# Performance work log

Measured on AMD Instinct MI355X. Metric: run time of the kernel, lower is better.

The kernel has to match this reference:

```python
import jax, jax.numpy as jnp
import numpy as np

D_MODEL, D_STATE, D_CONV, EXPAND, N_HEADS = 1024, 64, 4, 2, 8
D_INNER = EXPAND * D_MODEL
D_HEAD = D_INNER // N_HEADS
B, T = 2, 2048
EPS = 1e-6


def setup_inputs() -> dict:
    key = jax.random.key(0)
    ks = jax.random.split(key, 12)
    s = 0.02
    return {
        "x": jax.random.normal(ks[0], (B, T, D_MODEL), jnp.float32),
        "norm_w": jnp.ones((D_MODEL,), jnp.float32),
        "in_w": jax.random.normal(ks[1], (2 * D_INNER, D_MODEL), jnp.float32) * s,
        "conv_w": jax.random.normal(ks[2], (D_INNER, 1, D_CONV), jnp.float32) * s,
        "conv_b": jnp.zeros((D_INNER,), jnp.float32),
        "A_log": jax.random.normal(ks[3], (N_HEADS,), jnp.float32),
        "B_w": jax.random.normal(ks[4], (N_HEADS * D_STATE, D_INNER), jnp.float32) * s,
        "C_w": jax.random.normal(ks[5], (N_HEADS * D_STATE, D_INNER), jnp.float32) * s,
        "dt_w": jax.random.normal(ks[6], (N_HEADS, D_INNER), jnp.float32) * s,
        "dt_b": jnp.zeros((N_HEADS,), jnp.float32),
        "D": jnp.ones((N_HEADS,), jnp.float32),
        "out_w": jax.random.normal(ks[7], (D_MODEL, D_INNER), jnp.float32) * s,
    }


def _rmsnorm(x, w):
    var = jnp.mean(jnp.square(x), axis=-1, keepdims=True)
    return x * jax.lax.rsqrt(var + EPS) * w


def _silu(x):
    return x * jax.nn.sigmoid(x)


def reference(x, norm_w, in_w, conv_w, conv_b, A_log, B_w, C_w, dt_w, dt_b, D, out_w):
    residual = x
    xn = _rmsnorm(x, norm_w)
    xz = xn @ in_w.T                                   # (B,T,2*D_INNER)
    x_ssm, z = jnp.split(xz, 2, axis=-1)

    # causal depthwise conv1d (torch pads both sides by K-1 then slices [:T] == left pad only)
    xc = jnp.transpose(x_ssm, (0, 2, 1))               # (B,C,T)
    xc = jax.lax.conv_general_dilated(
        xc, conv_w, window_strides=(1,), padding=[(D_CONV - 1, 0)],
        feature_group_count=D_INNER,
        dimension_numbers=("NCH", "OIH", "NCH"))
    xc = xc + conv_b[None, :, None]
    x_ssm = _silu(jnp.transpose(xc, (0, 2, 1)))        # (B,T,D_INNER)

    dt = jax.nn.softplus(x_ssm @ dt_w.T + dt_b)        # (B,T,H)
    Bm = (x_ssm @ B_w.T).reshape(B, T, N_HEADS, D_STATE)
    Cm = (x_ssm @ C_w.T).reshape(B, T, N_HEADS, D_STATE)
    xh = x_ssm.reshape(B, T, N_HEADS, D_HEAD)
    A = -jnp.exp(A_log)                                # (H,)

    # time-major for scan
    dt_t = jnp.transpose(dt, (1, 0, 2))                # (T,B,H)
    B_t = jnp.transpose(Bm, (1, 0, 2, 3))              # (T,B,H,N)
    C_t = jnp.transpose(Cm, (1, 0, 2, 3))
    x_t = jnp.transpose(xh, (1, 0, 2, 3))              # (T,B,H,D)

    def step(h, inp):
        dtt, bt, ct, xt = inp
        dA = jnp.exp(dtt * A)[..., None, None]         # (B,H,1,1)
        h = dA * h + dtt[..., None, None] * bt[..., :, None] * xt[..., None, :]
        y = jnp.einsum("bhn,bhnd->bhd", ct, h)
        return h, y

    h0 = jnp.zeros((B, N_HEADS, D_STATE, D_HEAD), x.dtype)
    _, ys = jax.lax.scan(step, h0, (dt_t, B_t, C_t, x_t))  # ys: (T,B,H,D)
    y = jnp.transpose(ys, (1, 0, 2, 3))                # (B,T,H,D)
    y = y + xh * D[None, None, :, None]
    y = y.reshape(B, T, D_INNER)
    y = y * _silu(z)
    out = y @ out_w.T
    return residual + out
```

## Files before the change

### kernel.cpp

```cpp
#include <hip/hip_runtime.h>
#include <hip/hip_bf16.h>
#include <math.h>

#define D_MODEL 1024
#define D_STATE 64
#define D_CONV  4
#define D_INNER 2048
#define N_HEADS 8
#define D_HEAD  256
#define BATCH   2
#define SEQ     2048
#define ROWS    (BATCH*SEQ)
#define NCHUNK  32
#define EPS     1e-6f

typedef __attribute__((ext_vector_type(2))) unsigned short ushort2v;
typedef __attribute__((ext_vector_type(4))) unsigned short ushort4v;
typedef __attribute__((ext_vector_type(8))) unsigned short ushort8v;
typedef __attribute__((ext_vector_type(8))) short short8v;
typedef __attribute__((ext_vector_type(4))) float f32x4;

__device__ __forceinline__ float silu_f(float x){ return x / (1.0f + __expf(-x)); }
__device__ __forceinline__ float softplus_f(float x){ return (x > 20.0f) ? x : log1pf(__expf(x)); }
__device__ __forceinline__ float bf2f(unsigned short u){
    union { unsigned int i; float f; } v; v.i = ((unsigned int)u) << 16; return v.f;
}
__device__ __forceinline__ unsigned short f2bf_bits(float f){
    __hip_bfloat16 h = __float2bfloat16(f);
    return *(unsigned short*)&h;
}
__device__ __forceinline__ void gload_lds16(const void* g, void* l){
    __builtin_amdgcn_global_load_lds((const __attribute__((address_space(1))) void*)g,
                                     (__attribute__((address_space(3))) void*)l, 16, 0, 0);
}
__device__ __forceinline__ void vmw(int n){
    switch(n){
        case 0:  asm volatile("s_waitcnt vmcnt(0)"  ::: "memory"); break;
        case 2:  asm volatile("s_waitcnt vmcnt(2)"  ::: "memory"); break;
        case 3:  asm volatile("s_waitcnt vmcnt(3)"  ::: "memory"); break;
        case 4:  asm volatile("s_waitcnt vmcnt(4)"  ::: "memory"); break;
        case 6:  asm volatile("s_waitcnt vmcnt(6)"  ::: "memory"); break;
        case 8:  asm volatile("s_waitcnt vmcnt(8)"  ::: "memory"); break;
        default: asm volatile("s_waitcnt vmcnt(0)"  ::: "memory"); break;
    }
}

__global__ __launch_bounds__(256) void prep_kernel(const float* __restrict__ in_w,
                                                   const float* __restrict__ out_w,
                                                   const float* __restrict__ B_w,
                                                   const float* __restrict__ C_w,
                                                   unsigned short* __restrict__ inw_bf,
                                                   unsigned short* __restrict__ outw_bf,
                                                   unsigned short* __restrict__ BCw_bf){
    int i = blockIdx.x * 256 + threadIdx.x;
    const float* src; unsigned short* dst; int j;
    if (i < 1048576)      { src = in_w;  dst = inw_bf;            j = i; }
    else if (i < 1572864) { src = out_w; dst = outw_bf;           j = i - 1048576; }
    else if (i < 1835008) { src = B_w;   dst = BCw_bf;            j = i - 1572864; }
    else                  { src = C_w;   dst = BCw_bf + 1048576;  j = i - 1835008; }
    float4 v = ((const float4*)src)[j];
    ushort4v o;
    o[0] = f2bf_bits(v.x); o[1] = f2bf_bits(v.y);
    o[2] = f2bf_bits(v.z); o[3] = f2bf_bits(v.w);
    ((ushort4v*)dst)[j] = o;
}

__global__ __launch_bounds__(256) void rmsnorm_kernel(const float* __restrict__ x,
                                                      const float* __restrict__ w,
                                                      unsigned short* __restrict__ xn){
    int row = blockIdx.x;
    int tid = threadIdx.x;
    const float4* xr = (const float4*)(x + (size_t)row * D_MODEL);
    float4 a = xr[tid];
    float ss = a.x*a.x + a.y*a.y + a.z*a.z + a.w*a.w;
    #pragma unroll
    for (int i = 1; i < 64; i <<= 1) ss += __shfl_xor(ss, i);
    __shared__ float red[4];
    int lane = tid & 63, wid = tid >> 6;
    if (lane == 0) red[wid] = ss;
    __syncthreads();
    float tot = red[0] + red[1] + red[2] + red[3];
    float scale = rsqrtf(tot * (1.0f / D_MODEL) + EPS);
    float4 wv = ((const float4*)w)[tid];
    ushort4v o;
    o[0] = f2bf_bits(a.x * scale * wv.x);
    o[1] = f2bf_bits(a.y * scale * wv.y);
    o[2] = f2bf_bits(a.z * scale * wv.z);
    o[3] = f2bf_bits(a.w * scale * wv.w);
    ((ushort4v*)(xn + (size_t)row * D_MODEL))[tid] = o;
}

__global__ __launch_bounds__(512) void gemm_in512(const unsigned short* __restrict__ A,
                                                  const unsigned short* __restrict__ W,
                                                  unsigned short* __restrict__ Cout0,
                                                  unsigned short* __restrict__ Cout1){
    const int K = D_MODEL;
    __shared__ unsigned short As[2][256*32];
    __shared__ unsigned short Bs[2][128*32];
    int tid = threadIdx.x;
    int bid = blockIdx.x;
    int x = bid & 7;
    int r = bid >> 3;
    int m0 = ((x & 3)*4 + (r >> 4)) * 256;
    int n0 = ((x >> 2)*16 + (r & 15)) * 128;

    int lane = tid & 63;
    int w = tid >> 6;
    int wrow = w >> 1, wcol = w & 1;
    f32x4 acc[4][4];
    #pragma unroll
    for (int i = 0; i < 4; ++i)
        #pragma unroll
        for (int j = 0; j < 4; ++j) acc[i][j] = (f32x4){0.f,0.f,0.f,0.f};

    int g0 = tid >> 3, s0 = tid & 7;
    int swz0 = (s0*16) ^ ((g0&7)<<4);
    int r0 = 2*g0 + (swz0 >> 6);
    int c0e = (swz0 & 63) >> 1;
    const unsigned short* aS0 = A + (size_t)(m0 + r0)*K + c0e;
    const unsigned short* aS1 = aS0 + (size_t)128*K;
    const unsigned short* bS0 = W + (size_t)(n0 + r0)*K + c0e;

    int frow = lane & 15;
    int fkb  = (lane >> 4) * 16;
    int offA[4], offB[4];
    #pragma unroll
    for (int m = 0; m < 4; ++m){
        int rr = wrow*64 + m*16 + frow;
        int lb = (rr&1)*64 + fkb;
        offA[m] = (rr>>1)*128 + (lb ^ (((rr>>1)&7)<<4));
    }
    #pragma unroll
    for (int n = 0; n < 4; ++n){
        int rr = wcol*64 + n*16 + frow;
        int lb = (rr&1)*64 + fkb;
        offB[n] = (rr>>1)*128 + (lb ^ (((rr>>1)&7)<<4));
    }

    #define STAGE(buf, k0) do{ \
        gload_lds16(aS0 + (k0), &As[buf][(size_t)tid*8]); \
        gload_lds16(aS1 + (k0), &As[buf][(size_t)(tid+512)*8]); \
        gload_lds16(bS0 + (k0), &Bs[buf][(size_t)tid*8]); \
    }while(0)

    #define COMPUTE(buf, tt) do{ \
        short8v af[4], bf[4]; \
        _Pragma("unroll") \
        for (int m = 0; m < 4; ++m) af[m] = *(const short8v*)((const char*)As[buf] + offA[m]); \
        _Pragma("unroll") \
        for (int n = 0; n < 4; ++n) bf[n] = *(const short8v*)((const char*)Bs[buf] + offB[n]); \
        asm volatile("s_waitcnt lgkmcnt(0)" ::: "memory"); \
        __builtin_amdgcn_sched_barrier(0); \
        __builtin_amdgcn_s_barrier(); \
        if ((tt) + 2 < NT) STAGE(buf, (size_t)((tt)+2)*32); \
        _Pragma("unroll") \
        for (int m = 0; m < 4; ++m) \
            _Pragma("unroll") \
            for (int n = 0; n < 4; ++n) \
                acc[m][n] = __builtin_amdgcn_mfma_f32_16x16x32_bf16(af[m], bf[n], acc[m][n], 0, 0, 0); \
    }while(0)

    int NT = K >> 5;
    STAGE(0, 0);
    STAGE(1, 32);
    int t = 0;
    for (; t < NT-1; ++t){
        vmw(3);
        __builtin_amdgcn_sched_barrier(0);
        __builtin_amdgcn_s_barrier();
        COMPUTE(t & 1, t);
    }
    {
        vmw(0);
        __builtin_amdgcn_sched_barrier(0);
        __builtin_amdgcn_s_barrier();
        COMPUTE(t & 1, t);
    }
    #undef COMPUTE
    #undef STAGE

    int rrow = (lane >> 4) * 4;
    int rcol = lane & 15;
    unsigned short* outp;
    int colbase;
    if (n0 < 2048){ outp = Cout0; colbase = n0; }
    else          { outp = Cout1; colbase = n0 - 2048; }
    #pragma unroll
    for (int m = 0; m < 4; ++m)
        #pragma unroll
        for (int n = 0; n < 4; ++n){
            int cc = colbase + wcol*64 + n*16 + rcol;
            #pragma unroll
            for (int i = 0; i < 4; ++i){
                int rr = m0 + wrow*64 + m*16 + rrow + i;
                outp[(size_t)rr*2048 + cc] = f2bf_bits(acc[m][n][i]);
            }
        }
}

template<int MODE>
__global__ __launch_bounds__(512) void gemm_k2048(const unsigned short* __restrict__ A,
                                                  const unsigned short* __restrict__ W,
                                                  void* __restrict__ Cout0,
                                                  const float* __restrict__ resid,
                                                  int M, int N, int K){
    __shared__ unsigned short As[4][128*32];
    __shared__ unsigned short Bs[4][128*32];
    int tid = threadIdx.x;
    int bid = blockIdx.x;
    int x = bid & 7;
    int sw = bid >> 3;
    int ml = sw >> 2;
    int nl = sw & 3;
    int m0 = ((x & 3)*8 + ml) * 128;
    int n0 = (((x >> 2)*4) + nl) * 128;

    int lane = tid & 63;
    int w = tid >> 6;
    int wrow = w >> 2, wcol = w & 3;
    f32x4 acc[4][2];
    #pragma unroll
    for (int i = 0; i < 4; ++i)
        #pragma unroll
        for (int j = 0; j < 2; ++j) acc[i][j] = (f32x4){0.f,0.f,0.f,0.f};

    int g0 = tid >> 3, s0 = tid & 7;
    int swz0 = (s0*16) ^ ((g0&7)<<4);
    int r0 = 2*g0 + (swz0 >> 6);
    int c0e = (swz0 & 63) >> 1;
    const unsigned short* aS = A + (size_t)(m0 + r0)*K + c0e;
    const unsigned short* bS = W + (size_t)(n0 + r0)*K + c0e;

    int frow = lane & 15;
    int fkb  = (lane >> 4) * 16;
    int offA[4], offB[2];
    #pragma unroll
    for (int m = 0; m < 4; ++m){
        int r = wrow*64 + m*16 + frow;
        int lb = (r&1)*64 + fkb;
        offA[m] = (r>>1)*128 + (lb ^ (((r>>1)&7)<<4));
    }
    #pragma unroll
    for (int n = 0; n < 2; ++n){
        int r = wcol*32 + n*16 + frow;
        int lb = (r&1)*64 + fkb;
        offB[n] = (r>>1)*128 + (lb ^ (((r>>1)&7)<<4));
    }

    #define STAGE(buf, k0) do{ \
        gload_lds16(aS + (k0), &As[buf][(size_t)tid*8]); \
        gload_lds16(bS + (k0), &Bs[buf][(size_t)tid*8]); \
    }while(0)

    #define COMPUTE(buf, tt) do{ \
        short8v af[4], bf[2]; \
        _Pragma("unroll") \
        for (int m = 0; m < 4; ++m) af[m] = *(const short8v*)((const char*)As[buf] + offA[m]); \
        _Pragma("unroll") \
        for (int n = 0; n < 2; ++n) bf[n] = *(const short8v*)((const char*)Bs[buf] + offB[n]); \
        asm volatile("s_waitcnt lgkmcnt(0)" ::: "memory"); \
        __builtin_amdgcn_sched_barrier(0); \
        __builtin_amdgcn_s_barrier(); \
        if ((tt) + 4 < NT) STAGE(buf, (size_t)((tt)+4)*32); \
        _Pragma("unroll") \
        for (int m = 0; m < 4; ++m) \
            _Pragma("unroll") \
            for (int n = 0; n < 2; ++n) \
                acc[m][n] = __builtin_amdgcn_mfma_f32_16x16x32_bf16(af[m], bf[n], acc[m][n], 0, 0, 0); \
    }while(0)

    int NT = K >> 5;
    #pragma unroll
    for (int p = 0; p < 4; ++p) STAGE(p, (size_t)p*32);

    int t = 0;
    for (; t < NT-3; ++t){
        vmw(6);
        __builtin_amdgcn_sched_barrier(0);
        __builtin_amdgcn_s_barrier();
        COMPUTE(t & 3, t);
    }
    #pragma unroll
    for (int j = 2; j >= 0; --j){
        vmw(2*j);
        __builtin_amdgcn_sched_barrier(0);
        __builtin_amdgcn_s_barrier();
        COMPUTE(t & 3, t);
        ++t;
    }
    #undef COMPUTE
    #undef STAGE

    int rrow = (lane >> 4) * 4;
    int rcol = lane & 15;
    if (MODE == 2){
        float* Co = (float*)Cout0;
        #pragma unroll
        for (int m = 0; m < 4; ++m)
            #pragma unroll
            for (int n = 0; n < 2; ++n){
                int cc = n0 + wcol*32 + n*16 + rcol;
                #pragma unroll
                for (int i = 0; i < 4; ++i){
                    int rr = m0 + wrow*64 + m*16 + rrow + i;
                    Co[(size_t)rr*N + cc] = acc[m][n][i] + resid[(size_t)rr*N + cc];
                }
            }
    } else {
        unsigned short* outp = (unsigned short*)Cout0;
        #pragma unroll
        for (int m = 0; m < 4; ++m)
            #pragma unroll
            for (int n = 0; n < 2; ++n){
                int cc = n0 + wcol*32 + n*16 + rcol;
                #pragma unroll
                for (int i = 0; i < 4; ++i){
                    int rr = m0 + wrow*64 + m*16 + rrow + i;
                    outp[(size_t)rr*N + cc] = f2bf_bits(acc[m][n][i]);
                }
            }
    }
}

__global__ __launch_bounds__(256) void conv_dt_kernel(const unsigned short* __restrict__ xp,
                                                      const float* __restrict__ cw,
                                                      const float* __restrict__ cb,
                                                      const float* __restrict__ dt_w,
                                                      const float* __restrict__ dt_b,
                                                      unsigned short* __restrict__ xs,
                                                      float* __restrict__ dt){
    int bid = blockIdx.x;
    int r0 = ((bid & 7)*64 + (bid >> 3)) * 8;
    int t0 = r0 & (SEQ - 1);
    int tid = threadIdx.x;
    int c8 = tid*8;

    float4 cwv[8];
    #pragma unroll
    for (int k = 0; k < 8; ++k) cwv[k] = ((const float4*)cw)[c8 + k];
    float cbv[8];
    {
        float4 cb0 = ((const float4*)cb)[tid*2];
        float4 cb1 = ((const float4*)cb)[tid*2+1];
        cbv[0]=cb0.x; cbv[1]=cb0.y; cbv[2]=cb0.z; cbv[3]=cb0.w;
        cbv[4]=cb1.x; cbv[5]=cb1.y; cbv[6]=cb1.z; cbv[7]=cb1.w;
    }
    float4 dw[8][2];
    #pragma unroll
    for (int h = 0; h < 8; ++h){
        dw[h][0] = *(const float4*)(dt_w + (size_t)h*D_INNER + c8);
        dw[h][1] = *(const float4*)(dt_w + (size_t)h*D_INNER + c8 + 4);
    }

    ushort8v zero8 = {0,0,0,0,0,0,0,0};
    ushort8v xm3, xm2, xm1, cur, nxt;
    if (t0 >= 3){
        xm3 = *(const ushort8v*)(xp + (size_t)(r0-3)*D_INNER + c8);
        xm2 = *(const ushort8v*)(xp + (size_t)(r0-2)*D_INNER + c8);
        xm1 = *(const ushort8v*)(xp + (size_t)(r0-1)*D_INNER + c8);
    } else {
        xm3 = zero8; xm2 = zero8; xm1 = zero8;
    }
    cur = *(const ushort8v*)(xp + (size_t)r0*D_INNER + c8);

    __shared__ float redl[8][32][9];
    int lane = tid & 63, wid = tid >> 6;
    int sub = lane >> 3, hsel = lane & 7;

    #pragma unroll
    for (int i = 0; i < 8; ++i){
        if (i < 7) nxt = *(const ushort8v*)(xp + (size_t)(r0+i+1)*D_INNER + c8);
        float xsv[8];
        ushort8v o;
        #pragma unroll
        for (int k = 0; k < 8; ++k){
            float a = cbv[k]
                    + bf2f(xm3[k])*cwv[k].x
                    + bf2f(xm2[k])*cwv[k].y
                    + bf2f(xm1[k])*cwv[k].z
                    + bf2f(cur[k])*cwv[k].w;
            xsv[k] = silu_f(a);
            o[k] = f2bf_bits(xsv[k]);
        }
        *(ushort8v*)(xs + (size_t)(r0+i)*D_INNER + c8) = o;

        float p[8];
        #pragma unroll
        for (int h = 0; h < 8; ++h){
            p[h] = xsv[0]*dw[h][0].x + xsv[1]*dw[h][0].y + xsv[2]*dw[h][0].z + xsv[3]*dw[h][0].w
                 + xsv[4]*dw[h][1].x + xsv[5]*dw[h][1].y + xsv[6]*dw[h][1].z + xsv[7]*dw[h][1].w;
        }
        #pragma unroll
        for (int h = 0; h < 8; ++h){
            p[h] += __shfl_xor(p[h], 1);
            p[h] += __shfl_xor(p[h], 2);
            p[h] += __shfl_xor(p[h], 4);
        }
        redl[i][wid*8 + sub][hsel] = p[hsel];
        xm3 = xm2; xm2 = xm1; xm1 = cur; cur = nxt;
    }
    __syncthreads();
    {
        int row  = tid >> 5;
        int quad = (tid >> 3) & 3;
        int h    = tid & 7;
        float v = 0.f;
        #pragma unroll
        for (int q = 0; q < 8; ++q) v += redl[row][quad*8 + q][h];
        v += __shfl_xor(v, 8);
        v += __shfl_xor(v, 16);
        if (quad == 0)
            dt[(size_t)(r0+row)*N_HEADS + h] = softplus_f(v + dt_b[h]);
    }
}

__global__ __launch_bounds__(256) void xdT_kernel(const unsigned short* __restrict__ xs,
                                                  const float* __restrict__ dtb,
                                                  const float* __restrict__ A_log,
                                                  unsigned short* __restrict__ xdT,
                                                  float* __restrict__ cums){
    int ct = blockIdx.x, cd = blockIdx.y, bh = blockIdx.z;
    int b = bh >> 3, h = bh & 7;
    __shared__ unsigned short sT[64*68];
    int tid = threadIdx.x;
    if (cd == 0 && tid < 64){
        int t = ct*64 + tid;
        float Ah = -__expf(A_log[h]);
        float a = dtb[(size_t)(b*SEQ + t)*N_HEADS + h] * Ah;
        #pragma unroll
        for (int i = 1; i < 64; i <<= 1){
            float v = __shfl_up(a, i);
            if (tid >= i) a += v;
        }
        cums[((size_t)bh)*SEQ + t] = a;
    }
    #pragma unroll
    for (int it = 0; it < 2; ++it){
        int l = tid + it*256;
        int tl = l >> 3, seg = l & 7;
        int row = b*SEQ + ct*64 + tl;
        ushort8v v = *(const ushort8v*)(xs + (size_t)row*D_INNER + h*D_HEAD + cd*64 + seg*8);
        float dtv = dtb[(size_t)row*N_HEADS + h];
        ushort4v lo, hi;
        #pragma unroll
        for (int j = 0; j < 4; ++j){
            lo[j] = f2bf_bits(bf2f(v[j]) * dtv);
            hi[j] = f2bf_bits(bf2f(v[j+4]) * dtv);
        }
        *(ushort4v*)((char*)sT + tl*136 + seg*16)     = lo;
        *(ushort4v*)((char*)sT + tl*136 + seg*16 + 8) = hi;
    }
    __syncthreads();
    #pragma unroll
    for (int it = 0; it < 2; ++it){
        int l = tid + it*256;
        int dl = l >> 3, tseg = l & 7;
        ushort8v o;
        #pragma unroll
        for (int j = 0; j < 8; ++j) o[j] = sT[(tseg*8 + j)*68 + dl];
        *(ushort8v*)(xdT + ((size_t)bh*D_HEAD + cd*64 + dl)*SEQ + ct*64 + tseg*8) = o;
    }
}

__global__ __launch_bounds__(256) void chunk_state_mfma(const unsigned short* __restrict__ xdT,
                                                        const unsigned short* __restrict__ BCm,
                                                        const float* __restrict__ cums,
                                                        unsigned short* __restrict__ HSb){
    int c = blockIdx.x;
    int by = blockIdx.y;
    int h = by >> 1, dh = by & 1;
    int b = blockIdx.z;
    int tid = threadIdx.x;
    int bh = b*N_HEADS + h;
    int t0 = c*64;
    __shared__ unsigned short sX[128*64];
    __shared__ unsigned short sBdT[64*72];
    __shared__ float sdec[64];
    if (tid < 64)
        sdec[tid] = __expf(cums[(size_t)bh*SEQ + t0 + 63] - cums[(size_t)bh*SEQ + t0 + tid]);
    const unsigned short* xb = xdT + ((size_t)bh*D_HEAD + dh*128)*SEQ + t0;
    #pragma unroll
    for (int it = 0; it < 4; ++it){
        int l = tid + it*256;
        int d = l >> 3, seg = l & 7;
        gload_lds16(xb + (size_t)d*SEQ + (((seg*16) ^ ((d&7)<<4)) >> 1),
                    (char*)sX + (size_t)l*16);
    }
    __syncthreads();
    #pragma unroll
    for (int it = 0; it < 2; ++it){
        int l = tid + it*256;
        int tl = l >> 3, seg = l & 7;
        ushort8v bv = *(const ushort8v*)(BCm + (size_t)(b*SEQ + t0 + tl)*1024 + h*64 + seg*8);
        float dec = sdec[tl];
        #pragma unroll
        for (int j = 0; j < 8; ++j)
            sBdT[(seg*8 + j)*72 + tl] = f2bf_bits(bf2f(bv[j]) * dec);
    }
    __syncthreads();

    int lane = tid & 63, w = tid >> 6;
    int d0 = w*32;
    int fr = lane & 15, fk = (lane >> 4)*8;
    f32x4 acc[2][4];
    #pragma unroll
    for (int i = 0; i < 2; ++i)
        #pragma unroll
        for (int j = 0; j < 4; ++j) acc[i][j] = (f32x4){0.f,0.f,0.f,0.f};
    short8v af[2][2], bg[4][2];
    #pragma unroll
    for (int m = 0; m < 2; ++m)
        #pragma unroll
        for (int k = 0; k < 2; ++k){
            int d = d0 + m*16 + fr;
            af[m][k] = *(const short8v*)((const char*)sX + (size_t)d*128 + (((k*32+fk)*2) ^ ((d&7)<<4)));
        }
    #pragma unroll
    for (int n = 0; n < 4; ++n)
        #pragma unroll
        for (int k = 0; k < 2; ++k)
            bg[n][k] = *(const short8v*)(sBdT + (size_t)(n*16 + fr)*72 + k*32 + fk);
    #pragma unroll
    for (int k = 0; k < 2; ++k)
        #pragma unroll
        for (int m = 0; m < 2; ++m)
            #pragma unroll
            for (int n = 0; n < 4; ++n)
                acc[m][n] = __builtin_amdgcn_mfma_f32_16x16x32_bf16(af[m][k], bg[n][k], acc[m][n], 0, 0, 0);

    unsigned short* out = HSb + ((size_t)bh*NCHUNK + c)*16384 + (size_t)dh*128*64;
    int rr = (lane >> 4)*4, rc = lane & 15;
    #pragma unroll
    for (int m = 0; m < 2; ++m)
        #pragma unroll
        for (int n = 0; n < 4; ++n)
            #pragma unroll
            for (int i = 0; i < 4; ++i)
                out[(size_t)(d0 + m*16 + rr + i)*64 + n*16 + rc] = f2bf_bits(acc[m][n][i]);
}

__global__ __launch_bounds__(256) void state_pass_kernel(const float* __restrict__ cums,
                                                         unsigned short* __restrict__ HSb){
    int e2 = blockIdx.x*256 + threadIdx.x;
    int bh = blockIdx.y;
    float Hx = 0.f, Hy = 0.f;
    ushort2v* p = (ushort2v*)(HSb + (size_t)bh*NCHUNK*16384) + e2;
    const float* cp = cums + (size_t)bh*SEQ + 63;
    for (int c = 0; c < NCHUNK; ++c){
        float Pc = __expf(cp[(size_t)c*64]);
        ushort2v s = *p;
        float sx = bf2f(s[0]), sy = bf2f(s[1]);
        ushort2v hold;
        hold[0] = f2bf_bits(Hx); hold[1] = f2bf_bits(Hy);
        *p = hold;
        Hx = fmaf(Pc, Hx, sx);
        Hy = fmaf(Pc, Hy, sy);
        p += 8192;
    }
}

__global__ __launch_bounds__(256) void chunk_out_mfma(const unsigned short* __restrict__ xs,
                                                      const unsigned short* __restrict__ z,
                                                      const unsigned short* __restrict__ BCm,
                                                      const unsigned short* __restrict__ xdT,
                                                      const float* __restrict__ cums,
                                                      const unsigned short* __restrict__ HSb,
                                                      const float* __restrict__ Dp,
                                                      unsigned short* __restrict__ y){
    int c = blockIdx.x;
    int by = blockIdx.y;
    int h = by >> 1, dh = by & 1;
    int b = blockIdx.z;
    int tid = threadIdx.x;
    int bh = b*N_HEADS + h;
    int t0 = c*64;
    __shared__ unsigned short regA[128*64];
    __shared__ unsigned short sW[64*64];
    __shared__ unsigned short sCd[64*64];
    __shared__ float scum[64];
    unsigned short* Craw = regA;
    unsigned short* Braw = regA + 64*64;

    if (tid < 64) scum[tid] = cums[(size_t)bh*SEQ + t0 + tid];
    #pragma unroll
    for (int it = 0; it < 2; ++it){
        int l = tid + it*256;
        int tl = l >> 3, seg = l & 7;
        size_t rowoff = (size_t)(b*SEQ + t0 + tl)*1024 + h*64;
        int soff = ((seg*16) ^ ((tl&7)<<4)) >> 1;
        gload_lds16(BCm + rowoff + 512 + soff, (char*)Craw + (size_t)l*16);
        gload_lds16(BCm + rowoff + soff,       (char*)Braw + (size_t)l*16);
    }
    __syncthreads();

    int lane = tid & 63, w = tid >> 6;
    int fr = lane & 15, fk = (lane >> 4)*8;
    int rr = (lane >> 4)*4, rc = lane & 15;

    int wr = w >> 1, wc = w & 1;
    f32x4 g[2][2];
    #pragma unroll
    for (int i = 0; i < 2; ++i)
        #pragma unroll
        for (int j = 0; j < 2; ++j) g[i][j] = (f32x4){0.f,0.f,0.f,0.f};
    {
        short8v ca[2][2], bb[2][2];
        #pragma unroll
        for (int m = 0; m < 2; ++m)
            #pragma unroll
            for (int k = 0; k < 2; ++k){
                int t = wr*32 + m*16 + fr;
                ca[m][k] = *(const short8v*)((const char*)Craw + (size_t)t*128 + (((k*32+fk)*2) ^ ((t&7)<<4)));
            }
        #pragma unroll
        for (int n = 0; n < 2; ++n)
            #pragma unroll
            for (int k = 0; k < 2; ++k){
                int s = wc*32 + n*16 + fr;
                bb[n][k] = *(const short8v*)((const char*)Braw + (size_t)s*128 + (((k*32+fk)*2) ^ ((s&7)<<4)));
            }
        #pragma unroll
        for (int k = 0; k < 2; ++k)
            #pragma unroll
            for (int m = 0; m < 2; ++m)
                #pragma unroll
                for (int n = 0; n < 2; ++n)
                    g[m][n] = __builtin_amdgcn_mfma_f32_16x16x32_bf16(ca[m][k], bb[n][k], g[m][n], 0, 0, 0);
    }
    #pragma unroll
    for (int m = 0; m < 2; ++m)
        #pragma unroll
        for (int n = 0; n < 2; ++n)
            #pragma unroll
            for (int i = 0; i < 4; ++i){
                int t = wr*32 + m*16 + rr + i;
                int s = wc*32 + n*16 + rc;
                float wv = (s <= t) ? __expf(scum[t] - scum[s]) * g[m][n][i] : 0.f;
                *(unsigned short*)((char*)sW + (size_t)t*128 + ((s*2) ^ ((t&7)<<4))) = f2bf_bits(wv);
            }
    {
        int tl = tid >> 2, sg = tid & 3;
        float ef = __expf(scum[tl]);
        #pragma unroll
        for (int q = 0; q < 2; ++q){
            int off = ((sg*32 + q*16)) ^ ((tl&7)<<4);
            ushort8v cv = *(const ushort8v*)((const char*)Craw + (size_t)tl*128 + off);
            ushort8v ov;
            #pragma unroll
            for (int j = 0; j < 8; ++j) ov[j] = f2bf_bits(bf2f(cv[j]) * ef);
            *(ushort8v*)((char*)sCd + (size_t)tl*128 + off) = ov;
        }
    }
    __syncthreads();

    const unsigned short* xb = xdT + ((size_t)bh*D_HEAD + dh*128)*SEQ + t0;
    #pragma unroll
    for (int it = 0; it < 4; ++it){
        int l = tid + it*256;
        int d = l >> 3, seg = l & 7;
        gload_lds16(xb + (size_t)d*SEQ + (((seg*16) ^ ((d&7)<<4)) >> 1),
                    (char*)regA + (size_t)l*16);
    }
    __syncthreads();

    int d0 = w*32;
    f32x4 acc[4][2];
    #pragma unroll
    for (int i = 0; i < 4; ++i)
        #pragma unroll
        for (int j = 0; j < 2; ++j) acc[i][j] = (f32x4){0.f,0.f,0.f,0.f};
    {
        short8v aw[4][2], xd[2][2];
        #pragma unroll
        for (int m = 0; m < 4; ++m)
            #pragma unroll
            for (int k = 0; k < 2; ++k){
                int t = m*16 + fr;
                aw[m][k] = *(const short8v*)((const char*)sW + (size_t)t*128 + (((k*32+fk)*2) ^ ((t&7)<<4)));
            }
        #pragma unroll
        for (int n = 0; n < 2; ++n)
            #pragma unroll
            for (int k = 0; k < 2; ++k){
                int d = d0 + n*16 + fr;
                xd[n][k] = *(const short8v*)((const char*)regA + (size_t)d*128 + (((k*32+fk)*2) ^ ((d&7)<<4)));
            }
        #pragma unroll
        for (int k = 0; k < 2; ++k)
            #pragma unroll
            for (int m = 0; m < 4; ++m)
                #pragma unroll
                for (int n = 0; n < 2; ++n)
                    acc[m][n] = __builtin_amdgcn_mfma_f32_16x16x32_bf16(aw[m][k], xd[n][k], acc[m][n], 0, 0, 0);
    }
    __syncthreads();

    const unsigned short* hb = HSb + ((size_t)bh*NCHUNK + c)*16384 + (size_t)dh*128*64;
    #pragma unroll
    for (int it = 0; it < 4; ++it){
        int l = tid + it*256;
        int d = l >> 3, seg = l & 7;
        gload_lds16(hb + (size_t)d*64 + (((seg*16) ^ ((d&7)<<4)) >> 1),
                    (char*)regA + (size_t)l*16);
    }
    __syncthreads();

    {
        short8v aw[4][2], ht[2][2];
        #pragma unroll
        for (int m = 0; m < 4; ++m)
            #pragma unroll
            for (int k = 0; k < 2; ++k){
                int t = m*16 + fr;
                aw[m][k] = *(const short8v*)((const char*)sCd + (size_t)t*128 + (((k*32+fk)*2) ^ ((t&7)<<4)));
            }
        #pragma unroll
        for (int n = 0; n < 2; ++n)
            #pragma unroll
            for (int k = 0; k < 2; ++k){
                int d = d0 + n*16 + fr;
                ht[n][k] = *(const short8v*)((const char*)regA + (size_t)d*128 + (((k*32+fk)*2) ^ ((d&7)<<4)));
            }
        #pragma unroll
        for (int k = 0; k < 2; ++k)
            #pragma unroll
            for (int m = 0; m < 4; ++m)
                #pragma unroll
                for (int n = 0; n < 2; ++n)
                    acc[m][n] = __builtin_amdgcn_mfma_f32_16x16x32_bf16(aw[m][k], ht[n][k], acc[m][n], 0, 0, 0);
    }

    float Dh = Dp[h];
    #pragma unroll
    for (int m = 0; m < 4; ++m)
        #pragma unroll
        for (int n = 0; n < 2; ++n)
            #pragma unroll
            for (int i = 0; i < 4; ++i){
                int t = m*16 + rr + i;
                int d = dh*128 + d0 + n*16 + rc;
                size_t off = (size_t)(b*SEQ + t0 + t)*D_INNER + h*D_HEAD + d;
                float val = acc[m][n][i] + Dh * bf2f(xs[off]);
                y[off] = f2bf_bits(val * silu_f(bf2f(z[off])));
            }
}

extern "C" void kernel_launch(void* const* d_in, const int* in_sizes, int n_in,
                              void* d_out, int out_size, void* d_ws, size_t ws_size,
                              hipStream_t stream){
    const float* x      = (const float*)d_in[0];
    const float* norm_w = (const float*)d_in[1];
    const float* in_w   = (const float*)d_in[2];
    const float* conv_w = (const float*)d_in[3];
    const float* conv_b = (const float*)d_in[4];
    const float* A_log  = (const float*)d_in[5];
    const float* B_w    = (const float*)d_in[6];
    const float* C_w    = (const float*)d_in[7];
    const float* dt_w   = (const float*)d_in[8];
    const float* dt_b   = (const float*)d_in[9];
    const float* Dp     = (const float*)d_in[10];
    const float* out_w  = (const float*)d_in[11];
    float* out = (float*)d_out;

    char* ws = (char*)d_ws;
    const size_t MB = 1048576ull;
    unsigned short* xpre_bf = (unsigned short*)(ws);
    unsigned short* y_bf    = xpre_bf;
    unsigned short* z_bf    = (unsigned short*)(ws + 16*MB);
    unsigned short* xs_bf   = (unsigned short*)(ws + 32*MB);
    unsigned short* inw_bf  = (unsigned short*)(ws + 48*MB);
    unsigned short* xdT     = (unsigned short*)(ws + 48*MB);
    unsigned short* HSb     = (unsigned short*)(ws + 64*MB);
    unsigned short* BCm     = (unsigned short*)(ws + 80*MB);
    unsigned short* outw_bf = (unsigned short*)(ws + 88*MB);
    unsigned short* BCw_bf  = (unsigned short*)(ws + 92*MB);
    unsigned short* xn_bf   = (unsigned short*)(ws + 96*MB);
    float*          dtb     = (float*)(ws + 104*MB);
    float*          cums    = (float*)(ws + 104*MB + 131072);

    prep_kernel<<<8192, 256, 0, stream>>>(in_w, out_w, B_w, C_w,
                                          inw_bf, outw_bf, BCw_bf);

    rmsnorm_kernel<<<ROWS, 256, 0, stream>>>(x, norm_w, xn_bf);

    gemm_in512<<<512, 512, 0, stream>>>(xn_bf, inw_bf, xpre_bf, z_bf);

    conv_dt_kernel<<<512, 256, 0, stream>>>(xpre_bf, conv_w, conv_b, dt_w, dt_b, xs_bf, dtb);

    gemm_k2048<0><<<256, 512, 0, stream>>>(xs_bf, BCw_bf, BCm, nullptr,
        ROWS, 1024, D_INNER);

    xdT_kernel<<<dim3(SEQ/64, D_HEAD/64, BATCH*N_HEADS), 256, 0, stream>>>(xs_bf, dtb, A_log, xdT, cums);

    chunk_state_mfma<<<dim3(NCHUNK, N_HEADS*2, BATCH), 256, 0, stream>>>(xdT, BCm, cums, HSb);

    state_pass_kernel<<<dim3(32, BATCH*N_HEADS), 256, 0, stream>>>(cums, HSb);

    chunk_out_mfma<<<dim3(NCHUNK, N_HEADS*2, BATCH), 256, 0, stream>>>(xs_bf, z_bf, BCm, xdT, cums, HSb, Dp, y_bf);

    gemm_k2048<2><<<256, 512, 0, stream>>>(y_bf, outw_bf, out, x,
        ROWS, D_MODEL, D_INNER);
}
```

Before: 173.8 us.

## Fold dt projection into B/C GEMM as extra padded columns

```diff
diff --git a/kernel.cpp b/kernel.cpp
--- a/kernel.cpp
+++ b/kernel.cpp
@@ -12,6 +12,7 @@
 #define SEQ     2048
 #define ROWS    (BATCH*SEQ)
 #define NCHUNK  32
+#define BCN     1152
 #define EPS     1e-6f
 
 typedef __attribute__((ext_vector_type(2))) unsigned short ushort2v;
@@ -40,7 +41,6 @@
         case 3:  asm volatile("s_waitcnt vmcnt(3)"  ::: "memory"); break;
         case 4:  asm volatile("s_waitcnt vmcnt(4)"  ::: "memory"); break;
         case 6:  asm volatile("s_waitcnt vmcnt(6)"  ::: "memory"); break;
-        case 8:  asm volatile("s_waitcnt vmcnt(8)"  ::: "memory"); break;
         default: asm volatile("s_waitcnt vmcnt(0)"  ::: "memory"); break;
     }
 }
@@ -49,6 +49,7 @@
                                                    const float* __restrict__ out_w,
                                                    const float* __restrict__ B_w,
                                                    const float* __restrict__ C_w,
+                                                   const float* __restrict__ dt_w,
                                                    unsigned short* __restrict__ inw_bf,
                                                    unsigned short* __restrict__ outw_bf,
                                                    unsigned short* __restrict__ BCw_bf){
@@ -57,7 +58,20 @@
     if (i < 1048576)      { src = in_w;  dst = inw_bf;            j = i; }
     else if (i < 1572864) { src = out_w; dst = outw_bf;           j = i - 1048576; }
     else if (i < 1835008) { src = B_w;   dst = BCw_bf;            j = i - 1572864; }
-    else                  { src = C_w;   dst = BCw_bf + 1048576;  j = i - 1835008; }
+    else if (i < 2097152) { src = C_w;   dst = BCw_bf + 1048576;  j = i - 1835008; }
+    else {
+        int k = i - 2097152;
+        int drow = k >> 9;
+        int col4 = k & 511;
+        ushort4v o = {0,0,0,0};
+        if (drow < 8){
+            float4 v = ((const float4*)(dt_w + (size_t)drow*D_INNER))[col4];
+            o[0] = f2bf_bits(v.x); o[1] = f2bf_bits(v.y);
+            o[2] = f2bf_bits(v.z); o[3] = f2bf_bits(v.w);
+        }
+        ((ushort4v*)(BCw_bf + (size_t)(1024 + drow)*D_INNER))[col4] = o;
+        return;
+    }
     float4 v = ((const float4*)src)[j];
     ushort4v o;
     o[0] = f2bf_bits(v.x); o[1] = f2bf_bits(v.y);
@@ -198,7 +212,7 @@
         }
 }
 
-template<int MODE>
+template<int MODE, int MAP>
 __global__ __launch_bounds__(512) void gemm_k2048(const unsigned short* __restrict__ A,
                                                   const unsigned short* __restrict__ W,
                                                   void* __restrict__ Cout0,
@@ -208,12 +222,17 @@
     __shared__ unsigned short Bs[4][128*32];
     int tid = threadIdx.x;
     int bid = blockIdx.x;
-    int x = bid & 7;
-    int sw = bid >> 3;
-    int ml = sw >> 2;
-    int nl = sw & 3;
-    int m0 = ((x & 3)*8 + ml) * 128;
-    int n0 = (((x >> 2)*4) + nl) * 128;
+    int m0, n0;
+    if (MAP == 0){
+        int x = bid & 7, sw = bid >> 3;
+        int ml = sw >> 2, nl = sw & 3;
+        m0 = ((x & 3)*8 + ml) * 128;
+        n0 = (((x >> 2)*4) + nl) * 128;
+    } else {
+        int x = bid & 7, sw = bid >> 3;
+        m0 = (x*4 + sw/9) * 128;
+        n0 = (sw % 9) * 128;
+    }
 
     int lane = tid & 63;
     int w = tid >> 6;
@@ -322,100 +341,46 @@
     }
 }
 
-__global__ __launch_bounds__(256) void conv_dt_kernel(const unsigned short* __restrict__ xp,
-                                                      const float* __restrict__ cw,
-                                                      const float* __restrict__ cb,
-                                                      const float* __restrict__ dt_w,
-                                                      const float* __restrict__ dt_b,
-                                                      unsigned short* __restrict__ xs,
-                                                      float* __restrict__ dt){
+__global__ __launch_bounds__(256) void conv_silu_kernel(const unsigned short* __restrict__ xp,
+                                                        const float* __restrict__ cw,
+                                                        const float* __restrict__ cb,
+                                                        unsigned short* __restrict__ xs){
     int bid = blockIdx.x;
-    int r0 = ((bid & 7)*64 + (bid >> 3)) * 8;
-    int t0 = r0 & (SEQ - 1);
+    int r = (bid & 7)*512 + (bid >> 3);
+    int t = r & (SEQ - 1);
     int tid = threadIdx.x;
     int c8 = tid*8;
 
+    ushort8v zero8 = {0,0,0,0,0,0,0,0};
+    ushort8v v[4];
+    #pragma unroll
+    for (int jj = 0; jj < 4; ++jj){
+        int tt = t - 3 + jj;
+        v[jj] = (tt >= 0) ? *(const ushort8v*)(xp + (size_t)(r-3+jj)*D_INNER + c8) : zero8;
+    }
     float4 cwv[8];
     #pragma unroll
     for (int k = 0; k < 8; ++k) cwv[k] = ((const float4*)cw)[c8 + k];
-    float cbv[8];
-    {
-        float4 cb0 = ((const float4*)cb)[tid*2];
-        float4 cb1 = ((const float4*)cb)[tid*2+1];
-        cbv[0]=cb0.x; cbv[1]=cb0.y; cbv[2]=cb0.z; cbv[3]=cb0.w;
-        cbv[4]=cb1.x; cbv[5]=cb1.y; cbv[6]=cb1.z; cbv[7]=cb1.w;
-    }
-    float4 dw[8][2];
-    #pragma unroll
-    for (int h = 0; h < 8; ++h){
-        dw[h][0] = *(const float4*)(dt_w + (size_t)h*D_INNER + c8);
-        dw[h][1] = *(const float4*)(dt_w + (size_t)h*D_INNER + c8 + 4);
-    }
-
-    ushort8v zero8 = {0,0,0,0,0,0,0,0};
-    ushort8v xm3, xm2, xm1, cur, nxt;
-    if (t0 >= 3){
-        xm3 = *(const ushort8v*)(xp + (size_t)(r0-3)*D_INNER + c8);
-        xm2 = *(const ushort8v*)(xp + (size_t)(r0-2)*D_INNER + c8);
-        xm1 = *(const ushort8v*)(xp + (size_t)(r0-1)*D_INNER + c8);
-    } else {
-        xm3 = zero8; xm2 = zero8; xm1 = zero8;
-    }
-    cur = *(const ushort8v*)(xp + (size_t)r0*D_INNER + c8);
-
-    __shared__ float redl[8][32][9];
-    int lane = tid & 63, wid = tid >> 6;
-    int sub = lane >> 3, hsel = lane & 7;
-
-    #pragma unroll
-    for (int i = 0; i < 8; ++i){
-        if (i < 7) nxt = *(const ushort8v*)(xp + (size_t)(r0+i+1)*D_INNER + c8);
-        float xsv[8];
-        ushort8v o;
-        #pragma unroll
-        for (int k = 0; k < 8; ++k){
-            float a = cbv[k]
-                    + bf2f(xm3[k])*cwv[k].x
-                    + bf2f(xm2[k])*cwv[k].y
-                    + bf2f(xm1[k])*cwv[k].z
-                    + bf2f(cur[k])*cwv[k].w;
-            xsv[k] = silu_f(a);
-            o[k] = f2bf_bits(xsv[k]);
-        }
-        *(ushort8v*)(xs + (size_t)(r0+i)*D_INNER + c8) = o;
-
-        float p[8];
-        #pragma unroll
-        for (int h = 0; h < 8; ++h){
-            p[h] = xsv[0]*dw[h][0].x + xsv[1]*dw[h][0].y + xsv[2]*dw[h][0].z + xsv[3]*dw[h][0].w
-                 + xsv[4]*dw[h][1].x + xsv[5]*dw[h][1].y + xsv[6]*dw[h][1].z + xsv[7]*dw[h][1].w;
-        }
-        #pragma unroll
-        for (int h = 0; h < 8; ++h){
-            p[h] += __shfl_xor(p[h], 1);
-            p[h] += __shfl_xor(p[h], 2);
-            p[h] += __shfl_xor(p[h], 4);
-        }
-        redl[i][wid*8 + sub][hsel] = p[hsel];
-        xm3 = xm2; xm2 = xm1; xm1 = cur; cur = nxt;
-    }
-    __syncthreads();
-    {
-        int row  = tid >> 5;
-        int quad = (tid >> 3) & 3;
-        int h    = tid & 7;
-        float v = 0.f;
-        #pragma unroll
-        for (int q = 0; q < 8; ++q) v += redl[row][quad*8 + q][h];
-        v += __shfl_xor(v, 8);
-        v += __shfl_xor(v, 16);
-        if (quad == 0)
-            dt[(size_t)(r0+row)*N_HEADS + h] = softplus_f(v + dt_b[h]);
-    }
+    float4 cb0 = ((const float4*)cb)[tid*2];
+    float4 cb1 = ((const float4*)cb)[tid*2+1];
+    float cbv[8] = {cb0.x,cb0.y,cb0.z,cb0.w,cb1.x,cb1.y,cb1.z,cb1.w};
+
+    ushort8v o;
+    #pragma unroll
+    for (int k = 0; k < 8; ++k){
+        float a = cbv[k]
+                + bf2f(v[0][k])*cwv[k].x
+                + bf2f(v[1][k])*cwv[k].y
+                + bf2f(v[2][k])*cwv[k].z
+                + bf2f(v[3][k])*cwv[k].w;
+        o[k] = f2bf_bits(silu_f(a));
+    }
+    *(ushort8v*)(xs + (size_t)r*D_INNER + c8) = o;
 }
 
 __global__ __launch_bounds__(256) void xdT_kernel(const unsigned short* __restrict__ xs,
-                                                  const float* __restrict__ dtb,
+                                                  const unsigned short* __restrict__ BCm,
+                                                  const float* __restrict__ dt_b,
                                                   const float* __restrict__ A_log,
                                                   unsigned short* __restrict__ xdT,
                                                   float* __restrict__ cums){
@@ -423,10 +388,12 @@
     int b = bh >> 3, h = bh & 7;
     __shared__ unsigned short sT[64*68];
     int tid = threadIdx.x;
+    float dtbh = dt_b[h];
     if (cd == 0 && tid < 64){
         int t = ct*64 + tid;
         float Ah = -__expf(A_log[h]);
-        float a = dtb[(size_t)(b*SEQ + t)*N_HEADS + h] * Ah;
+        float raw = bf2f(BCm[(size_t)(b*SEQ + t)*BCN + 1024 + h]);
+        float a = softplus_f(raw + dtbh) * Ah;
         #pragma unroll
         for (int i = 1; i < 64; i <<= 1){
             float v = __shfl_up(a, i);
@@ -440,7 +407,8 @@
         int tl = l >> 3, seg = l & 7;
         int row = b*SEQ + ct*64 + tl;
         ushort8v v = *(const ushort8v*)(xs + (size_t)row*D_INNER + h*D_HEAD + cd*64 + seg*8);
-        float dtv = dtb[(size_t)row*N_HEADS + h];
+        float raw = bf2f(BCm[(size_t)row*BCN + 1024 + h]);
+        float dtv = softplus_f(raw + dtbh);
         ushort4v lo, hi;
         #pragma unroll
         for (int j = 0; j < 4; ++j){
@@ -491,7 +459,7 @@
     for (int it = 0; it < 2; ++it){
         int l = tid + it*256;
         int tl = l >> 3, seg = l & 7;
-        ushort8v bv = *(const ushort8v*)(BCm + (size_t)(b*SEQ + t0 + tl)*1024 + h*64 + seg*8);
+        ushort8v bv = *(const ushort8v*)(BCm + (size_t)(b*SEQ + t0 + tl)*BCN + h*64 + seg*8);
         float dec = sdec[tl];
         #pragma unroll
         for (int j = 0; j < 8; ++j)
@@ -586,7 +554,7 @@
     for (int it = 0; it < 2; ++it){
         int l = tid + it*256;
         int tl = l >> 3, seg = l & 7;
-        size_t rowoff = (size_t)(b*SEQ + t0 + tl)*1024 + h*64;
+        size_t rowoff = (size_t)(b*SEQ + t0 + tl)*BCN + h*64;
         int soff = ((seg*16) ^ ((tl&7)<<4)) >> 1;
         gload_lds16(BCm + rowoff + 512 + soff, (char*)Craw + (size_t)l*16);
         gload_lds16(BCm + rowoff + soff,       (char*)Braw + (size_t)l*16);
@@ -772,25 +740,24 @@
     unsigned short* xdT     = (unsigned short*)(ws + 48*MB);
     unsigned short* HSb     = (unsigned short*)(ws + 64*MB);
     unsigned short* BCm     = (unsigned short*)(ws + 80*MB);
-    unsigned short* outw_bf = (unsigned short*)(ws + 88*MB);
-    unsigned short* BCw_bf  = (unsigned short*)(ws + 92*MB);
-    unsigned short* xn_bf   = (unsigned short*)(ws + 96*MB);
-    float*          dtb     = (float*)(ws + 104*MB);
-    float*          cums    = (float*)(ws + 104*MB + 131072);
-
-    prep_kernel<<<8192, 256, 0, stream>>>(in_w, out_w, B_w, C_w,
+    unsigned short* outw_bf = (unsigned short*)(ws + 90*MB);
+    unsigned short* xn_bf   = (unsigned short*)(ws + 94*MB);
+    unsigned short* BCw_bf  = (unsigned short*)(ws + 102*MB);
+    float*          cums    = (float*)(ws + 107*MB);
+
+    prep_kernel<<<8448, 256, 0, stream>>>(in_w, out_w, B_w, C_w, dt_w,
                                           inw_bf, outw_bf, BCw_bf);
 
     rmsnorm_kernel<<<ROWS, 256, 0, stream>>>(x, norm_w, xn_bf);
 
     gemm_in512<<<512, 512, 0, stream>>>(xn_bf, inw_bf, xpre_bf, z_bf);
 
-    conv_dt_kernel<<<512, 256, 0, stream>>>(xpre_bf, conv_w, conv_b, dt_w, dt_b, xs_bf, dtb);
-
-    gemm_k2048<0><<<256, 512, 0, stream>>>(xs_bf, BCw_bf, BCm, nullptr,
-        ROWS, 1024, D_INNER);
-
-    xdT_kernel<<<dim3(SEQ/64, D_HEAD/64, BATCH*N_HEADS), 256, 0, stream>>>(xs_bf, dtb, A_log, xdT, cums);
+    conv_silu_kernel<<<4096, 256, 0, stream>>>(xpre_bf, conv_w, conv_b, xs_bf);
+
+    gemm_k2048<0,1><<<288, 512, 0, stream>>>(xs_bf, BCw_bf, BCm, nullptr,
+        ROWS, BCN, D_INNER);
+
+    xdT_kernel<<<dim3(SEQ/64, D_HEAD/64, BATCH*N_HEADS), 256, 0, stream>>>(xs_bf, BCm, dt_b, A_log, xdT, cums);
 
     chunk_state_mfma<<<dim3(NCHUNK, N_HEADS*2, BATCH), 256, 0, stream>>>(xdT, BCm, cums, HSb);
 
@@ -798,6 +765,6 @@
 
     chunk_out_mfma<<<dim3(NCHUNK, N_HEADS*2, BATCH), 256, 0, stream>>>(xs_bf, z_bf, BCm, xdT, cums, HSb, Dp, y_bf);
 
-    gemm_k2048<2><<<256, 512, 0, stream>>>(y_bf, outw_bf, out, x,
+    gemm_k2048<2,0><<<256, 512, 0, stream>>>(y_bf, outw_bf, out, x,
         ROWS, D_MODEL, D_INNER);
 }
```

Result: slower. 182.5 us (+5.0%).
